# Kernel optimization log

Measured on AMD Instinct MI355X. Metric: run time of the kernel, lower is better.

Reference implementation:

```python
import jax, jax.numpy as jnp
import numpy as np

N = 500_000        # batch rows
K_OLD = 128        # old bins -> 129 edges
K_NEW = 100        # new bins -> 101 edges


def setup_inputs() -> dict:
    key = jax.random.key(0)
    logits = jax.random.normal(key, (N, K_OLD), dtype=jnp.float32)
    # strictly increasing edge grids (monotone, mismatched resolution)
    old_edges = jnp.linspace(0.0, 1.0, K_OLD + 1, dtype=jnp.float32)
    new_edges = jnp.linspace(0.0, 1.0, K_NEW + 1, dtype=jnp.float32)
    return {"logits": logits, "old_edges": old_edges, "new_edges": new_edges}


def reference(logits, old_edges, new_edges):
    # softmax over bins -> per-bin probability mass
    probs = jax.nn.softmax(logits, axis=-1)                      # [N, K_old]
    widths = old_edges[1:] - old_edges[:-1]                      # [K_old]
    density = probs / widths                                     # [N, K_old]
    # overlap[i, j] = length of intersection of old bin i with new bin j.
    # Equivalent to the per-new-bin mask/gather/sum loop in _rebin_pc:
    # bins with no strict overlap contribute exactly 0 after the clip.
    overlap = jnp.clip(
        jnp.minimum(old_edges[1:, None], new_edges[None, 1:])
        - jnp.maximum(old_edges[:-1, None], new_edges[None, :-1]),
        0.0,
    )                                                            # [K_old, K_new]
    rebinned = density @ overlap                                 # [N, K_new]
    eps = jnp.finfo(rebinned.dtype).tiny
    return jnp.log(rebinned + eps)
```

## Files before the change

kernel.cpp:

```cpp
#include <hip/hip_runtime.h>
#include <math.h>

#define KOLD 128
#define KNEW 100
#define GPB  8

#define META_OFF 1024
#define PE_OFF   2688
#define LDS_BYTES (PE_OFF + 4 * 4 * 128 * 8)

template <int CTRL, int ROWM>
__device__ __forceinline__ float dpp_add(float v) {
    int s = __builtin_amdgcn_update_dpp(0, __float_as_int(v), CTRL, ROWM, 0xf, true);
    return v + __int_as_float(s);
}
__device__ __forceinline__ float scan32(float v) {
    v = dpp_add<0x111, 0xf>(v);
    v = dpp_add<0x112, 0xf>(v);
    v = dpp_add<0x114, 0xf>(v);
    v = dpp_add<0x118, 0xf>(v);
    v = dpp_add<0x142, 0xa>(v);
    return v;
}
__device__ __forceinline__ float grp_total(float scanned, int half) {
    int t0 = __builtin_amdgcn_readlane(__float_as_int(scanned), 31);
    int t1 = __builtin_amdgcn_readlane(__float_as_int(scanned), 63);
    return __int_as_float(half ? t1 : t0);
}

__launch_bounds__(256, 8)
__global__ void rebin_k(const float* __restrict__ logits,
                        const float* __restrict__ oe,
                        const float* __restrict__ ne,
                        float* __restrict__ out, int nrows)
{
    __shared__ __align__(16) char lds[LDS_BYTES];
    int*   tmp_i = (int*)(lds + 0);
    float* tmp_t = (float*)(lds + 512);
    uint4* meta  = (uint4*)(lds + META_OFF);

    const int tid  = threadIdx.x;
    const int lane = tid & 63;
    const int wid  = tid >> 6;
    const int c    = lane & 31;
    const int half = lane >> 5;

    if (tid <= KNEW) {
        float e = ne[tid];
        int i = 0;
#pragma unroll
        for (int st = 64; st >= 1; st >>= 1) {
            int cand = i + st;
            if (cand <= KOLD - 1 && oe[cand] <= e) i = cand;
        }
        float a = oe[i], b = oe[i + 1];
        float tt = (e - a) / (b - a);
        tmp_i[tid] = i;
        tmp_t[tid] = fminf(fmaxf(tt, 0.f), 1.f);
    }
    __syncthreads();
    if (tid < KNEW) {
        uint4 m;
        m.x = (unsigned)(tmp_i[tid] * 8);
        m.y = __float_as_uint(tmp_t[tid]);
        m.z = (unsigned)(tmp_i[tid + 1] * 8);
        m.w = __float_as_uint(tmp_t[tid + 1]);
        meta[tid] = m;
    }
    __syncthreads();

    char* peW = lds + PE_OFF + wid * 4096;
    const int nm1 = nrows - 1;
    const int ngroups = (nrows + 15) >> 4;
    const float tiny = 1.1754943508222875e-38f;

#pragma unroll 1
    for (int k = 0; k < GPB; ++k) {
        const int grp = blockIdx.x * GPB + k;
        if (grp >= ngroups) break;
        const int wrow0 = grp * 16 + wid * 4;

        const size_t offA = (size_t)min(wrow0 + half, nm1) * KOLD + c * 4;
        const size_t offB = (size_t)min(wrow0 + 2 + half, nm1) * KOLD + c * 4;
        const float4 vA = *(const float4*)(logits + offA);
        const float4 vB = *(const float4*)(logits + offB);

        const float eA0 = __expf(fminf(fmaxf(vA.x, -80.f), 80.f));
        const float eA1 = __expf(fminf(fmaxf(vA.y, -80.f), 80.f));
        const float eA2 = __expf(fminf(fmaxf(vA.z, -80.f), 80.f));
        const float eA3 = __expf(fminf(fmaxf(vA.w, -80.f), 80.f));
        const float eB0 = __expf(fminf(fmaxf(vB.x, -80.f), 80.f));
        const float eB1 = __expf(fminf(fmaxf(vB.y, -80.f), 80.f));
        const float eB2 = __expf(fminf(fmaxf(vB.z, -80.f), 80.f));
        const float eB3 = __expf(fminf(fmaxf(vB.w, -80.f), 80.f));

        const float sA = (eA0 + eA1) + (eA2 + eA3);
        const float sB = (eB0 + eB1) + (eB2 + eB3);
        const float iA = scan32(sA);
        const float iB = scan32(sB);
        const float totA = grp_total(iA, half);
        const float totB = grp_total(iB, half);
        float rA = __builtin_amdgcn_rcpf(totA);
        float rB = __builtin_amdgcn_rcpf(totB);
        const float invA = rA * (2.0f - totA * rA);
        const float invB = rB * (2.0f - totB * rB);
        const float exA  = iA - sA;
        const float exB  = iB - sB;

        {
            float p0 = exA, p1 = p0 + eA0, p2 = p1 + eA1, p3 = p2 + eA2;
            char* base = peW + half * 1024 + c * 32;
            *(float4*)(base)      = make_float4(eA0 * invA, p0 * invA, eA1 * invA, p1 * invA);
            *(float4*)(base + 16) = make_float4(eA2 * invA, p2 * invA, eA3 * invA, p3 * invA);
        }
        {
            float p0 = exB, p1 = p0 + eB0, p2 = p1 + eB1, p3 = p2 + eB2;
            char* base = peW + (2 + half) * 1024 + c * 32;
            *(float4*)(base)      = make_float4(eB0 * invB, p0 * invB, eB1 * invB, p1 * invB);
            *(float4*)(base + 16) = make_float4(eB2 * invB, p2 * invB, eB3 * invB, p3 * invB);
        }
        asm volatile("s_waitcnt lgkmcnt(0)" ::: "memory");

        float* gbase = out + (size_t)wrow0 * KNEW;
        if (wrow0 + 4 <= nrows) {
#pragma unroll
            for (int it = 0; it < 7; ++it) {
                const int flat  = it * 64 + lane;
                const int flatc = flat < 399 ? flat : 399;
                const int r = (flatc * 5243) >> 19;
                const int j = flatc - r * 100;
                const uint4 mt = meta[j];
                const char* rowp = peW + r * 1024;
                const float2 ep0 = *(const float2*)(rowp + mt.x);
                const float2 ep1 = *(const float2*)(rowp + mt.z);
                const float F0 = fmaf(__uint_as_float(mt.y), ep0.x, ep0.y);
                const float F1 = fmaf(__uint_as_float(mt.w), ep1.x, ep1.y);
                const float v  = fmaxf(F1 - F0, 0.f) + tiny;
                if (flat < 400) gbase[flat] = __logf(v);
            }
        } else {
            long long liml = (long long)(nrows - wrow0) * KNEW;
            const int lim = liml > 400 ? 400 : (liml < 0 ? 0 : (int)liml);
#pragma unroll
            for (int it = 0; it < 7; ++it) {
                const int flat  = it * 64 + lane;
                const int flatc = flat < 399 ? flat : 399;
                const int r = (flatc * 5243) >> 19;
                const int j = flatc - r * 100;
                const uint4 mt = meta[j];
                const char* rowp = peW + r * 1024;
                const float2 ep0 = *(const float2*)(rowp + mt.x);
                const float2 ep1 = *(const float2*)(rowp + mt.z);
                const float F0 = fmaf(__uint_as_float(mt.y), ep0.x, ep0.y);
                const float F1 = fmaf(__uint_as_float(mt.w), ep1.x, ep1.y);
                const float v  = fmaxf(F1 - F0, 0.f) + tiny;
                if (flat < lim) gbase[flat] = __logf(v);
            }
        }
        asm volatile("" ::: "memory");
    }
}

extern "C" void kernel_launch(void* const* d_in, const int* in_sizes, int n_in,
                              void* d_out, int out_size, void* d_ws, size_t ws_size,
                              hipStream_t stream) {
    const float* logits = (const float*)d_in[0];
    const float* oe     = (const float*)d_in[1];
    const float* ne     = (const float*)d_in[2];
    float* out          = (float*)d_out;
    const int nrows     = in_sizes[0] / KOLD;

    const int ngroups = (nrows + 15) / 16;
    const int blocks  = (ngroups + GPB - 1) / GPB;
    rebin_k<<<blocks, 256, 0, stream>>>(logits, oe, ne, out, nrows);
}
```

Baseline: 99.33 us.

## Scatter CDF values at new edges directly from producer lanes, vectorize output

Each lane now precomputes which new-bin edges fall inside its four old bins, and writes only the interpolated cumulative probability at those edges (101 floats per row) into LDS, instead of writing the full prefix and element arrays for all 128 bins. The consumer phase then reads contiguous CDF values and writes four outputs per lane with float4 stores, which removes the per-output meta lookup and gather. This cuts LDS traffic and turns scalar global stores into vector stores. In exchange, the producer does extra select and FMA work per edge and assumes at most four new edges fall in any 4-bin chunk.

```diff
diff --git a/kernel.cpp b/kernel.cpp
--- a/kernel.cpp
+++ b/kernel.cpp
@@ -5,9 +5,10 @@
 #define KNEW 100
 #define GPB  8
 
-#define META_OFF 1024
-#define PE_OFF   2688
-#define LDS_BYTES (PE_OFF + 4 * 4 * 128 * 8)
+#define FT_OFF  1024
+#define ROW_B   416
+#define WAVE_B  (4 * ROW_B)
+#define LDS_BYTES (FT_OFF + 4 * WAVE_B)
 
 template <int CTRL, int ROWM>
 __device__ __forceinline__ float dpp_add(float v) {
@@ -37,7 +38,6 @@
     __shared__ __align__(16) char lds[LDS_BYTES];
     int*   tmp_i = (int*)(lds + 0);
     float* tmp_t = (float*)(lds + 512);
-    uint4* meta  = (uint4*)(lds + META_OFF);
 
     const int tid  = threadIdx.x;
     const int lane = tid & 63;
@@ -59,24 +59,35 @@
         tmp_t[tid] = fminf(fmaxf(tt, 0.f), 1.f);
     }
     __syncthreads();
-    if (tid < KNEW) {
-        uint4 m;
-        m.x = (unsigned)(tmp_i[tid] * 8);
-        m.y = __float_as_uint(tmp_t[tid]);
-        m.z = (unsigned)(tmp_i[tid + 1] * 8);
-        m.w = __float_as_uint(tmp_t[tid + 1]);
-        meta[tid] = m;
+
+    int k0 = 0;
+#pragma unroll
+    for (int st = 64; st >= 1; st >>= 1) {
+        int cand = k0 + st;
+        if (cand <= KNEW + 1 && tmp_i[cand - 1] < 4 * c) k0 = cand;
     }
-    __syncthreads();
+    unsigned kb[4];
+    float    te[4];
+    int      se[4];
+#pragma unroll
+    for (int e = 0; e < 4; ++e) {
+        int k  = k0 + e;
+        int kc = k <= KNEW ? k : KNEW;
+        int ib = tmp_i[kc];
+        bool ok = (k <= KNEW) && (ib < 4 * c + 4);
+        kb[e] = ok ? (unsigned)(k * 4) : 102u * 4u;
+        te[e] = ok ? tmp_t[kc] : 0.f;
+        se[e] = ok ? (ib - 4 * c) : 0;
+    }
 
-    char* peW = lds + PE_OFF + wid * 4096;
+    char* fW = lds + FT_OFF + wid * WAVE_B;
     const int nm1 = nrows - 1;
     const int ngroups = (nrows + 15) >> 4;
     const float tiny = 1.1754943508222875e-38f;
 
 #pragma unroll 1
-    for (int k = 0; k < GPB; ++k) {
-        const int grp = blockIdx.x * GPB + k;
+    for (int kg = 0; kg < GPB; ++kg) {
+        const int grp = blockIdx.x * GPB + kg;
         if (grp >= ngroups) break;
         const int wrow0 = grp * 16 + wid * 4;
 
@@ -85,77 +96,75 @@
         const float4 vA = *(const float4*)(logits + offA);
         const float4 vB = *(const float4*)(logits + offB);
 
-        const float eA0 = __expf(fminf(fmaxf(vA.x, -80.f), 80.f));
-        const float eA1 = __expf(fminf(fmaxf(vA.y, -80.f), 80.f));
-        const float eA2 = __expf(fminf(fmaxf(vA.z, -80.f), 80.f));
-        const float eA3 = __expf(fminf(fmaxf(vA.w, -80.f), 80.f));
-        const float eB0 = __expf(fminf(fmaxf(vB.x, -80.f), 80.f));
-        const float eB1 = __expf(fminf(fmaxf(vB.y, -80.f), 80.f));
-        const float eB2 = __expf(fminf(fmaxf(vB.z, -80.f), 80.f));
-        const float eB3 = __expf(fminf(fmaxf(vB.w, -80.f), 80.f));
-
-        const float sA = (eA0 + eA1) + (eA2 + eA3);
-        const float sB = (eB0 + eB1) + (eB2 + eB3);
-        const float iA = scan32(sA);
-        const float iB = scan32(sB);
-        const float totA = grp_total(iA, half);
-        const float totB = grp_total(iB, half);
-        float rA = __builtin_amdgcn_rcpf(totA);
-        float rB = __builtin_amdgcn_rcpf(totB);
-        const float invA = rA * (2.0f - totA * rA);
-        const float invB = rB * (2.0f - totB * rB);
-        const float exA  = iA - sA;
-        const float exB  = iB - sB;
-
         {
-            float p0 = exA, p1 = p0 + eA0, p2 = p1 + eA1, p3 = p2 + eA2;
-            char* base = peW + half * 1024 + c * 32;
-            *(float4*)(base)      = make_float4(eA0 * invA, p0 * invA, eA1 * invA, p1 * invA);
-            *(float4*)(base + 16) = make_float4(eA2 * invA, p2 * invA, eA3 * invA, p3 * invA);
+            const float e0 = __expf(fminf(fmaxf(vA.x, -80.f), 80.f));
+            const float e1 = __expf(fminf(fmaxf(vA.y, -80.f), 80.f));
+            const float e2 = __expf(fminf(fmaxf(vA.z, -80.f), 80.f));
+            const float e3 = __expf(fminf(fmaxf(vA.w, -80.f), 80.f));
+            const float sl = (e0 + e1) + (e2 + e3);
+            const float ic = scan32(sl);
+            const float tot = grp_total(ic, half);
+            float rc = __builtin_amdgcn_rcpf(tot);
+            const float inv = rc * (2.0f - tot * rc);
+            const float p0 = ic - sl;
+            const float p1 = p0 + e0, p2 = p1 + e1, p3 = p2 + e2;
+            char* frow = fW + half * ROW_B;
+#pragma unroll
+            for (int e = 0; e < 4; ++e) {
+                const float f0 = fmaf(te[e], e0, p0);
+                const float f1 = fmaf(te[e], e1, p1);
+                const float f2 = fmaf(te[e], e2, p2);
+                const float f3 = fmaf(te[e], e3, p3);
+                const float g01 = (se[e] & 1) ? f1 : f0;
+                const float g23 = (se[e] & 1) ? f3 : f2;
+                const float F   = (se[e] & 2) ? g23 : g01;
+                *(float*)(frow + kb[e]) = F * inv;
+            }
         }
         {
-            float p0 = exB, p1 = p0 + eB0, p2 = p1 + eB1, p3 = p2 + eB2;
-            char* base = peW + (2 + half) * 1024 + c * 32;
-            *(float4*)(base)      = make_float4(eB0 * invB, p0 * invB, eB1 * invB, p1 * invB);
-            *(float4*)(base + 16) = make_float4(eB2 * invB, p2 * invB, eB3 * invB, p3 * invB);
+            const float e0 = __expf(fminf(fmaxf(vB.x, -80.f), 80.f));
+            const float e1 = __expf(fminf(fmaxf(vB.y, -80.f), 80.f));
+            const float e2 = __expf(fminf(fmaxf(vB.z, -80.f), 80.f));
+            const float e3 = __expf(fminf(fmaxf(vB.w, -80.f), 80.f));
+            const float sl = (e0 + e1) + (e2 + e3);
+            const float ic = scan32(sl);
+            const float tot = grp_total(ic, half);
+            float rc = __builtin_amdgcn_rcpf(tot);
+            const float inv = rc * (2.0f - tot * rc);
+            const float p0 = ic - sl;
+            const float p1 = p0 + e0, p2 = p1 + e1, p3 = p2 + e2;
+            char* frow = fW + (2 + half) * ROW_B;
+#pragma unroll
+            for (int e = 0; e < 4; ++e) {
+                const float f0 = fmaf(te[e], e0, p0);
+                const float f1 = fmaf(te[e], e1, p1);
+                const float f2 = fmaf(te[e], e2, p2);
+                const float f3 = fmaf(te[e], e3, p3);
+                const float g01 = (se[e] & 1) ? f1 : f0;
+                const float g23 = (se[e] & 1) ? f3 : f2;
+                const float F   = (se[e] & 2) ? g23 : g01;
+                *(float*)(frow + kb[e]) = F * inv;
+            }
         }
         asm volatile("s_waitcnt lgkmcnt(0)" ::: "memory");
 
-        float* gbase = out + (size_t)wrow0 * KNEW;
-        if (wrow0 + 4 <= nrows) {
+        float* gout = out + (size_t)wrow0 * KNEW;
 #pragma unroll
-            for (int it = 0; it < 7; ++it) {
-                const int flat  = it * 64 + lane;
-                const int flatc = flat < 399 ? flat : 399;
-                const int r = (flatc * 5243) >> 19;
-                const int j = flatc - r * 100;
-                const uint4 mt = meta[j];
-                const char* rowp = peW + r * 1024;
-                const float2 ep0 = *(const float2*)(rowp + mt.x);
-                const float2 ep1 = *(const float2*)(rowp + mt.z);
-                const float F0 = fmaf(__uint_as_float(mt.y), ep0.x, ep0.y);
-                const float F1 = fmaf(__uint_as_float(mt.w), ep1.x, ep1.y);
-                const float v  = fmaxf(F1 - F0, 0.f) + tiny;
-                if (flat < 400) gbase[flat] = __logf(v);
-            }
-        } else {
-            long long liml = (long long)(nrows - wrow0) * KNEW;
-            const int lim = liml > 400 ? 400 : (liml < 0 ? 0 : (int)liml);
-#pragma unroll
-            for (int it = 0; it < 7; ++it) {
-                const int flat  = it * 64 + lane;
-                const int flatc = flat < 399 ? flat : 399;
-                const int r = (flatc * 5243) >> 19;
-                const int j = flatc - r * 100;
-                const uint4 mt = meta[j];
-                const char* rowp = peW + r * 1024;
-                const float2 ep0 = *(const float2*)(rowp + mt.x);
-                const float2 ep1 = *(const float2*)(rowp + mt.z);
-                const float F0 = fmaf(__uint_as_float(mt.y), ep0.x, ep0.y);
-                const float F1 = fmaf(__uint_as_float(mt.w), ep1.x, ep1.y);
-                const float v  = fmaxf(F1 - F0, 0.f) + tiny;
-                if (flat < lim) gbase[flat] = __logf(v);
-            }
+        for (int it = 0; it < 2; ++it) {
+            const int t  = it * 64 + lane;
+            const int tc = t < 100 ? t : 99;
+            const int r  = (tc * 41) >> 10;
+            const int q  = tc - r * 25;
+            const char* frow = fW + r * ROW_B + q * 16;
+            const float4 F4 = *(const float4*)(frow);
+            const float  F5 = *(const float*)(frow + 16);
+            float4 o;
+            o.x = __logf(fmaxf(F4.y - F4.x, 0.f) + tiny);
+            o.y = __logf(fmaxf(F4.z - F4.y, 0.f) + tiny);
+            o.z = __logf(fmaxf(F4.w - F4.z, 0.f) + tiny);
+            o.w = __logf(fmaxf(F5  - F4.w, 0.f) + tiny);
+            if (t < 100 && wrow0 + r < nrows)
+                *(float4*)(gout + r * KNEW + q * 4) = o;
         }
         asm volatile("" ::: "memory");
     }
```

Result: no change. 100.4 us (+1.1%).
